# Performance work log

Measured on AMD Instinct MI355X. Metric: run time of the kernel, lower is better.

Reference implementation:

```python
import jax, jax.numpy as jnp
import numpy as np

D = 64       # d_model (channel)
NHEAD = 8    # heads in nn.MultiheadAttention
PROTO = 16   # proto_size == num_queries
EPS = 1e-5


def _haar_filters():
    L = np.array([1.0, 1.0], np.float32) / np.float32(np.sqrt(2.0))
    H = np.array([-1.0, 1.0], np.float32) / np.float32(np.sqrt(2.0))
    # WavePool: LL, LH, HL, HH Haar filters (2x2, stride 2, depthwise)
    return [jnp.asarray(np.outer(a, b)) for (a, b) in ((L, L), (L, H), (H, L), (H, H))]


def _dw(x, k2d, stride):
    # depthwise conv with the SAME 2D filter per channel; x: [B,C,H,W]
    C = x.shape[1]
    k = jnp.tile(k2d[None, None], (C, 1, 1, 1)).astype(x.dtype)
    return jax.lax.conv_general_dilated(x, k, (stride, stride), 'VALID',
        dimension_numbers=('NCHW', 'OIHW', 'NCHW'), feature_group_count=C)


def _ln(x, g, b):
    m = jnp.mean(x, -1, keepdims=True)
    v = jnp.var(x, -1, keepdims=True)
    return (x - m) * jax.lax.rsqrt(v + EPS) * g + b


def _bn(x, g, b, m, v):
    # eval-mode BatchNorm2d, x: [B,C,H,W]
    sh = (1, -1, 1, 1)
    return (x - m.reshape(sh)) * jax.lax.rsqrt(v.reshape(sh) + EPS) * g.reshape(sh) + b.reshape(sh)


def _mscw(x, lw1, lb1, lw2, lb2, gw1, gb1, gw2, gb2):
    pool = jnp.mean(x, axis=1, keepdims=True)            # [B,1,C]
    loc = jax.nn.relu(x @ lw1.T + lb1) @ lw2.T + lb2
    glo = jax.nn.relu(pool @ gw1.T + gb1) @ gw2.T + gb2
    return jax.nn.sigmoid(loc + glo)


def _mha(q, k, v, w_in, b_in, w_out, b_out):
    # standard nn.MultiheadAttention (batch_first), q:[B,Nq,D], k/v:[B,Nk,D]
    B, Nq, d = q.shape
    dk = d // NHEAD
    qp = q @ w_in[:d].T + b_in[:d]
    kp = k @ w_in[d:2 * d].T + b_in[d:2 * d]
    vp = v @ w_in[2 * d:].T + b_in[2 * d:]
    split = lambda t: t.reshape(t.shape[0], t.shape[1], NHEAD, dk).transpose(0, 2, 1, 3)
    qh, kh, vh = split(qp), split(kp), split(vp)
    scores = jnp.einsum('bhqd,bhkd->bhqk', qh, kh) * (1.0 / np.sqrt(dk))
    attn = jax.nn.softmax(scores, axis=-1)
    o = jnp.einsum('bhqk,bhkd->bhqd', attn, vh).transpose(0, 2, 1, 3).reshape(B, Nq, d)
    return o @ w_out.T + b_out


def reference(tgt, memory, pos, query_pos,
              w_in, b_in, w_out, b_out,
              ln1_g, ln1_b, ln2_g, ln2_b,
              m1_lw1, m1_lb1, m1_lw2, m1_lb2, m1_gw1, m1_gb1, m1_gw2, m1_gb2,
              m2_lw1, m2_lb1, m2_lw2, m2_lb2, m2_gw1, m2_gb1, m2_gw2, m2_gb2,
              dw_w, bn1_g, bn1_b, bn1_m, bn1_v, pw_w, bn2_g, bn2_b, bn2_m, bn2_v,
              mheads_w):
    # CrossAttentionLayer.forward_post -> custom MultiheadAttention.forward
    query = (tgt + query_pos).transpose(1, 0, 2)   # [B,Nq,C]
    key = (memory + pos).transpose(1, 0, 2)        # [B,N1,C]
    value = memory.transpose(1, 0, 2)
    B, N1, C = value.shape
    hw = int(np.sqrt(N1))
    feat = key.transpose(0, 2, 1).reshape(B, C, hw, hw)
    fLL, fLH, fHL, fHH = _haar_filters()
    LL = _dw(feat, fLL, 2)
    LH = _dw(feat, fLH, 2)
    HL = _dw(feat, fHL, 2)
    HH = _dw(feat, fHH, 2)
    high = (HL + LH + HH).reshape(B, C, -1).transpose(0, 2, 1)  # [B,N1/4,C]
    low = LL.reshape(B, C, -1).transpose(0, 2, 1)
    wei = _mscw(high + low, m1_lw1, m1_lb1, m1_lw2, m1_lb2, m1_gw1, m1_gb1, m1_gw2, m1_gb2)
    fre = wei * high + low
    x1 = _mha(query, fre, fre, w_in, b_in, w_out, b_out)
    x1 = _ln(x1 + query, ln1_g, ln1_b)
    # DSConv3x3: depthwise 3x3 + BN + ReLU, then 1x1 + BN + ReLU
    y = jax.lax.conv_general_dilated(feat, dw_w, (1, 1), ((1, 1), (1, 1)),
        dimension_numbers=('NCHW', 'OIHW', 'NCHW'), feature_group_count=C)
    y = jax.nn.relu(_bn(y, bn1_g, bn1_b, bn1_m, bn1_v))
    y = jax.lax.conv_general_dilated(y, pw_w, (1, 1), 'VALID',
        dimension_numbers=('NCHW', 'OIHW', 'NCHW'))
    y = jax.nn.relu(_bn(y, bn2_g, bn2_b, bn2_m, bn2_v))
    featf = y.reshape(B, C, -1).transpose(0, 2, 1)          # [B,N1,C]
    mw = jax.nn.softmax(featf @ mheads_w.T, axis=1)          # softmax over tokens, [B,N1,P]
    protos = jnp.einsum('bnp,bnc->bpc', mw, key)             # [B,P,C]
    attn2 = _mscw(protos + query, m2_lw1, m2_lb1, m2_lw2, m2_lb2, m2_gw1, m2_gb1, m2_gw2, m2_gb2)
    x2 = _ln(query * attn2 + query, ln2_g, ln2_b)
    return (x1 + x2).transpose(1, 0, 2)                      # [Nq,B,C]


def setup_inputs() -> dict:
    key = jax.random.key(0)
    ks = iter(jax.random.split(key, 40))
    B, HW, NQ = 8, 128, PROTO
    N1 = HW * HW
    wn = lambda *s: jax.random.normal(next(ks), s, jnp.float32) * 0.05
    inp = {
        'tgt': jax.random.normal(next(ks), (NQ, B, D), jnp.float32),
        'memory': jax.random.normal(next(ks), (N1, B, D), jnp.float32),
        'pos': jax.random.normal(next(ks), (N1, B, D), jnp.float32),
        'query_pos': jax.random.normal(next(ks), (NQ, B, D), jnp.float32),
        'w_in': wn(3 * D, D), 'b_in': jnp.zeros((3 * D,), jnp.float32),
        'w_out': wn(D, D), 'b_out': jnp.zeros((D,), jnp.float32),
        'ln1_g': jnp.ones((D,), jnp.float32), 'ln1_b': jnp.zeros((D,), jnp.float32),
        'ln2_g': jnp.ones((D,), jnp.float32), 'ln2_b': jnp.zeros((D,), jnp.float32),
        'dw_w': wn(D, 1, 3, 3),
        'bn1_g': jnp.ones((D,), jnp.float32), 'bn1_b': jnp.zeros((D,), jnp.float32),
        'bn1_m': jnp.zeros((D,), jnp.float32), 'bn1_v': jnp.ones((D,), jnp.float32),
        'pw_w': wn(D, D, 1, 1),
        'bn2_g': jnp.ones((D,), jnp.float32), 'bn2_b': jnp.zeros((D,), jnp.float32),
        'bn2_m': jnp.zeros((D,), jnp.float32), 'bn2_v': jnp.ones((D,), jnp.float32),
        'mheads_w': wn(PROTO, D),
    }
    for pfx in ('m1', 'm2'):
        for br in ('l', 'g'):
            inp[f'{pfx}_{br}w1'] = wn(D, D)
            inp[f'{pfx}_{br}b1'] = jnp.zeros((D,), jnp.float32)
            inp[f'{pfx}_{br}w2'] = wn(D, D)
            inp[f'{pfx}_{br}b2'] = jnp.zeros((D,), jnp.float32)
    return inp
```

## Files before the change

### kernel.cpp

```cpp
#include <hip/hip_runtime.h>
#include <math.h>

#define N1 16384
#define N2 4096

#define OFF_KEY   0L
#define OFF_KPH   4194304L
#define OFF_VPH   5242880L
#define OFF_WB    6291456L
#define OFF_CST   6302208L
#define OFF_POOL  6331648L
#define OFF_PROT  6332160L
#define OFF_ZZ    6340352L
#define OFF_QP    6340480L
#define OFF_QB    6348672L
#define OFF_PART  6356864L

typedef __attribute__((ext_vector_type(8))) short bf16x8;
typedef __attribute__((ext_vector_type(4))) float floatx4;

#define MFMA16(a, b, c) __builtin_amdgcn_mfma_f32_16x16x32_bf16(a, b, c, 0, 0, 0)

__device__ __forceinline__ unsigned short f2bf(float f) {
    union { float f; unsigned u; } v; v.f = f;
    unsigned r = v.u + 0x7fffu + ((v.u >> 16) & 1u);
    return (unsigned short)(r >> 16);
}
__device__ __forceinline__ float bf2f(unsigned short s) {
    union { unsigned u; float f; } v; v.u = ((unsigned)s) << 16;
    return v.f;
}
__device__ __forceinline__ float sigmoidf_(float x) { return 1.f / (1.f + __expf(-x)); }
__device__ __forceinline__ bf16x8 ldg8b(const unsigned short* p) { return *(const bf16x8*)p; }
__device__ __forceinline__ void unpack8(uint4 v, float* f) {
    f[0] = bf2f((unsigned short)(v.x & 0xffff)); f[1] = bf2f((unsigned short)(v.x >> 16));
    f[2] = bf2f((unsigned short)(v.y & 0xffff)); f[3] = bf2f((unsigned short)(v.y >> 16));
    f[4] = bf2f((unsigned short)(v.z & 0xffff)); f[5] = bf2f((unsigned short)(v.z >> 16));
    f[6] = bf2f((unsigned short)(v.w & 0xffff)); f[7] = bf2f((unsigned short)(v.w >> 16));
}

__global__ __launch_bounds__(256) void k_prep(const float* __restrict__ m1lw1,
                                              const float* __restrict__ m1lw2,
                                              const float* __restrict__ w_in,
                                              const float* __restrict__ pw,
                                              const float* __restrict__ mh,
                                              const float* __restrict__ dw_w,
                                              const float* __restrict__ bn1_g, const float* __restrict__ bn1_b,
                                              const float* __restrict__ bn1_m, const float* __restrict__ bn1_v,
                                              const float* __restrict__ bn2_g, const float* __restrict__ bn2_b,
                                              const float* __restrict__ bn2_m, const float* __restrict__ bn2_v,
                                              const float* __restrict__ m1gw1, const float* __restrict__ m1gw2,
                                              const float* __restrict__ m2gw1, const float* __restrict__ m2gw2,
                                              const float* __restrict__ m2lw1, const float* __restrict__ m2lw2,
                                              const float* __restrict__ w_out,
                                              const float* __restrict__ tgt, const float* __restrict__ qpos,
                                              const float* __restrict__ b_in,
                                              unsigned short* __restrict__ wb,
                                              float* __restrict__ cst,
                                              float* __restrict__ qp, float* __restrict__ queryb) {
    int blk = blockIdx.x, tid = threadIdx.x;
    if (blk < 84) {
        int i = blk * 256 + tid;
        float v;
        if (i < 4096) v = m1lw1[i];
        else if (i < 8192) v = m1lw2[i - 4096];
        else if (i < 16384) v = w_in[4096 + (i - 8192)];
        else if (i < 20480) v = pw[i - 16384];
        else v = mh[i - 20480];
        wb[i] = f2bf(v);
    } else if (blk < 199) {
        int j = (blk - 84) * 256 + tid;
        float v;
        if (j < 576) {
            int k = j >> 6, c = j & 63;
            float s1 = bn1_g[c] * rsqrtf(bn1_v[c] + 1e-5f);
            v = dw_w[c * 9 + k] * s1;
        } else if (j < 640) {
            int c = j - 576;
            float s1 = bn1_g[c] * rsqrtf(bn1_v[c] + 1e-5f);
            v = bn1_b[c] - bn1_m[c] * s1;
        } else if (j < 704) {
            int c = j - 640;
            v = bn2_g[c] * rsqrtf(bn2_v[c] + 1e-5f);
        } else if (j < 768) {
            int c = j - 704;
            float s2 = bn2_g[c] * rsqrtf(bn2_v[c] + 1e-5f);
            v = bn2_b[c] - bn2_m[c] * s2;
        } else {
            int jj = j - 768;
            int m = jj >> 12, idx = jj & 4095;
            int sidx = (idx & 63) * 64 + (idx >> 6);
            const float* src;
            switch (m) {
                case 0: src = m1gw1; break;
                case 1: src = m1gw2; break;
                case 2: src = m2gw1; break;
                case 3: src = m2gw2; break;
                case 4: src = m2lw1; break;
                case 5: src = m2lw2; break;
                default: src = w_out; break;
            }
            v = src[sidx];
        }
        cst[j] = v;
    } else {
        __shared__ float qv[4][64];
        int g = tid >> 6, lane = tid & 63;
        int u = (blk - 199) * 4 + g;
        int b = u >> 4, q = u & 15;
        long src = ((long)q * 8 + b) * 64 + lane;
        float v = tgt[src] + qpos[src];
        qv[g][lane] = v;
        queryb[(b * 16 + q) * 64 + lane] = v;
        __syncthreads();
        float acc = b_in[lane];
        for (int cc = 0; cc < 64; cc++) acc += qv[g][cc] * w_in[lane * 64 + cc];
        qp[(b * 16 + q) * 64 + lane] = acc;
    }
}

__global__ __launch_bounds__(256) void k_key(const float* __restrict__ mem,
                                             const float* __restrict__ pos,
                                             unsigned short* __restrict__ key,
                                             float* __restrict__ pool1raw) {
    __shared__ float sh[16][64];
    int tid = threadIdx.x;
    int b = blockIdx.x >> 9;
    int n_base = (blockIdx.x & 511) * 32;
    int c8 = tid & 7, local_n = tid >> 3;
    int n = n_base + local_n;
    long s4 = ((long)n * 8 + b) * 16 + c8 * 2;
    float4 m0 = ((const float4*)mem)[s4], m1 = ((const float4*)mem)[s4 + 1];
    float4 p0 = ((const float4*)pos)[s4], p1 = ((const float4*)pos)[s4 + 1];
    float f[8];
    f[0] = m0.x + p0.x; f[1] = m0.y + p0.y; f[2] = m0.z + p0.z; f[3] = m0.w + p0.w;
    f[4] = m1.x + p1.x; f[5] = m1.y + p1.y; f[6] = m1.z + p1.z; f[7] = m1.w + p1.w;
    uint4 o;
    o.x = (unsigned)f2bf(f[0]) | ((unsigned)f2bf(f[1]) << 16);
    o.y = (unsigned)f2bf(f[2]) | ((unsigned)f2bf(f[3]) << 16);
    o.z = (unsigned)f2bf(f[4]) | ((unsigned)f2bf(f[5]) << 16);
    o.w = (unsigned)f2bf(f[6]) | ((unsigned)f2bf(f[7]) << 16);
    ((uint4*)key)[(long)(b * 16384 + n) * 8 + c8] = o;
    int parity = (n_base >> 7) & 1;
    if (parity) {
        if (local_n & 1) {
            #pragma unroll
            for (int j = 0; j < 8; j++) sh[local_n >> 1][c8 * 8 + j] = f[j];
        }
        __syncthreads();
        if (tid < 64) {
            float s = 0.f;
            #pragma unroll
            for (int k = 0; k < 16; k++) s += sh[k][tid];
            atomicAdd(pool1raw + b * 64 + tid, s);
        }
    }
}

__global__ __launch_bounds__(256) void k_mscw1(
        const unsigned short* __restrict__ keyb, const float* __restrict__ pool1raw,
        const float* __restrict__ lb1, const float* __restrict__ lb2,
        const float* __restrict__ gb1, const float* __restrict__ gb2,
        const float* __restrict__ b_in, const unsigned short* __restrict__ wb,
        const float* __restrict__ cst,
        unsigned short* __restrict__ kph, unsigned short* __restrict__ vph) {
    __shared__ __align__(16) short stage[256 * 72];
    __shared__ __align__(16) short hbuf[64 * 72];
    __shared__ __align__(16) short wbuf[64 * 72];
    __shared__ float parr[64], gtmp[64], gbuf[64];
    int tid = threadIdx.x;
    int w = tid >> 6, l = tid & 63;
    int b = blockIdx.x >> 6, tile = blockIdx.x & 63;
    int m0 = w * 16, trow = l & 15, oct = l >> 4;
    const float* gw1T = cst + 768;
    const float* gw2T = cst + 4864;
    if (tid < 64) parr[tid] = pool1raw[b * 64 + tid] * (2.0f / 4096.0f);
    const unsigned short* src = keyb + ((long)b * 16384 + tile * 256) * 64;
    #pragma unroll
    for (int k = 0; k < 8; k++) {
        int u = k * 256 + tid;
        int p = u >> 3, o = u & 7;
        uint4 v = *(const uint4*)(src + (long)u * 8);
        *(uint4*)(stage + p * 72 + o * 8) = v;
    }
    __syncthreads();
    if (tid < 64) {
        float a = gb1[tid];
        for (int cc = 0; cc < 64; cc++) a += parr[cc] * gw1T[cc * 64 + tid];
        gtmp[tid] = fmaxf(a, 0.f);
    }
    int j = m0 + trow;
    float x[16], S[16];
    bf16x8 ax[2];
    #pragma unroll
    for (int half = 0; half < 2; half++) {
        int o = oct + half * 4;
        uint4 fa4 = *(const uint4*)(stage + (2 * j) * 72 + o * 8);
        uint4 fb4 = *(const uint4*)(stage + (2 * j + 1) * 72 + o * 8);
        uint4 fc4 = *(const uint4*)(stage + (128 + 2 * j) * 72 + o * 8);
        uint4 fd4 = *(const uint4*)(stage + (129 + 2 * j) * 72 + o * 8);
        float A[8], B[8], C[8], D[8];
        unpack8(fa4, A); unpack8(fb4, B); unpack8(fc4, C); unpack8(fd4, D);
        #pragma unroll
        for (int jj = 0; jj < 8; jj++) {
            float xd = 2.f * D[jj];
            x[half * 8 + jj] = xd;
            S[half * 8 + jj] = 0.5f * (A[jj] + B[jj] + C[jj] + D[jj]);
            ax[half][jj] = (short)f2bf(xd);
        }
    }
    const unsigned short* w1b = wb;
    const unsigned short* w2b = wb + 4096;
    const unsigned short* wkb = wb + 8192;
    const unsigned short* wvb = wb + 12288;
    #pragma unroll
    for (int t4 = 0; t4 < 4; t4++) {
        int n = t4 * 16 + trow;
        float bias = lb1[n];
        floatx4 acc = {bias, bias, bias, bias};
        acc = MFMA16(ax[0], ldg8b(w1b + n * 64 + oct * 8), acc);
        acc = MFMA16(ax[1], ldg8b(w1b + n * 64 + 32 + oct * 8), acc);
        #pragma unroll
        for (int r = 0; r < 4; r++)
            hbuf[(m0 + oct * 4 + r) * 72 + n] = (short)f2bf(fmaxf(acc[r], 0.f));
    }
    __syncthreads();
    if (tid < 64) {
        float g = gb2[tid];
        for (int hh = 0; hh < 64; hh++) g += gtmp[hh] * gw2T[hh * 64 + tid];
        gbuf[tid] = g;
    }
    __syncthreads();
    {
        bf16x8 ah0 = *(const bf16x8*)(hbuf + (m0 + trow) * 72 + oct * 8);
        bf16x8 ah1 = *(const bf16x8*)(hbuf + (m0 + trow) * 72 + 32 + oct * 8);
        #pragma unroll
        for (int t4 = 0; t4 < 4; t4++) {
            int n = t4 * 16 + trow;
            float bias = lb2[n];
            floatx4 acc = {bias, bias, bias, bias};
            acc = MFMA16(ah0, ldg8b(w2b + n * 64 + oct * 8), acc);
            acc = MFMA16(ah1, ldg8b(w2b + n * 64 + 32 + oct * 8), acc);
            float g = gbuf[n];
            #pragma unroll
            for (int r = 0; r < 4; r++)
                wbuf[(m0 + oct * 4 + r) * 72 + n] = (short)f2bf(sigmoidf_(acc[r] + g));
        }
    }
    __syncthreads();
    bf16x8 af0, af1;
    {
        bf16x8 w0 = *(const bf16x8*)(wbuf + (m0 + trow) * 72 + oct * 8);
        bf16x8 w1v = *(const bf16x8*)(wbuf + (m0 + trow) * 72 + 32 + oct * 8);
        #pragma unroll
        for (int jj = 0; jj < 8; jj++) {
            float we0 = bf2f((unsigned short)w0[jj]);
            float we1 = bf2f((unsigned short)w1v[jj]);
            af0[jj] = (short)f2bf(we0 * x[jj] + (1.f - we0) * S[jj]);
            af1[jj] = (short)f2bf(we1 * x[8 + jj] + (1.f - we1) * S[8 + jj]);
        }
    }
    __syncthreads();
    short* kbuf = hbuf; short* vbuf = wbuf;
    #pragma unroll
    for (int t4 = 0; t4 < 4; t4++) {
        int ko = t4 * 16 + trow;
        float bk = b_in[64 + ko], bv = b_in[128 + ko];
        floatx4 ak = {bk, bk, bk, bk};
        floatx4 av = {bv, bv, bv, bv};
        ak = MFMA16(af0, ldg8b(wkb + ko * 64 + oct * 8), ak);
        ak = MFMA16(af1, ldg8b(wkb + ko * 64 + 32 + oct * 8), ak);
        av = MFMA16(af0, ldg8b(wvb + ko * 64 + oct * 8), av);
        av = MFMA16(af1, ldg8b(wvb + ko * 64 + 32 + oct * 8), av);
        #pragma unroll
        for (int r = 0; r < 4; r++) {
            int row = m0 + oct * 4 + r;
            kbuf[row * 72 + ko] = (short)f2bf(ak[r]);
            vbuf[row * 72 + ko] = (short)f2bf(av[r]);
        }
    }
    __syncthreads();
    for (int u = tid; u < 512; u += 256) {
        int h = u >> 6, tok = u & 63;
        uint4 kk = *(const uint4*)(kbuf + tok * 72 + h * 8);
        uint4 vv = *(const uint4*)(vbuf + tok * 72 + h * 8);
        long du = (long)(b * 8 + h) * 4096 + tile * 64 + tok;
        ((uint4*)kph)[du] = kk;
        ((uint4*)vph)[du] = vv;
    }
}

__global__ __launch_bounds__(512) void k_dsconv(
        const unsigned short* __restrict__ keyb,
        const unsigned short* __restrict__ wb,
        const float* __restrict__ cst,
        float* __restrict__ protos, float* __restrict__ Z) {
    __shared__ __align__(16) short stage[3 * 128 * 72];
    __shared__ __align__(16) short pbuf[16 * 136];
    __shared__ float cbuf[768];
    __shared__ float zred[8][16];
    int tid = threadIdx.x;
    int w = tid >> 6, l = tid & 63;
    int b = blockIdx.x >> 7, h = blockIdx.x & 127;
    int p0 = w * 16, pr = l & 15, oct = l >> 4;
    for (int k = tid; k < 768; k += 512) cbuf[k] = cst[k];
    const unsigned short* kb = keyb + (long)b * 1048576;
    #pragma unroll
    for (int r = 0; r < 3; r++) {
        int row = h - 1 + r;
        if ((unsigned)row < 128u) {
            const unsigned short* src = kb + (long)row * 8192;
            #pragma unroll
            for (int k = 0; k < 4; k++) {
                int u = k * 512 + tid;
                int p = u >> 3, o = u & 7;
                uint4 v = *(const uint4*)(src + (long)u * 8);
                *(uint4*)(stage + (r * 128 + p) * 72 + o * 8) = v;
            }
        } else {
            uint4 zz = {0u, 0u, 0u, 0u};
            #pragma unroll
            for (int k = 0; k < 4; k++) {
                int u = k * 512 + tid;
                int p = u >> 3, o = u & 7;
                *(uint4*)(stage + (r * 128 + p) * 72 + o * 8) = zz;
            }
        }
    }
    __syncthreads();
    float accf[2][8];
    #pragma unroll
    for (int half = 0; half < 2; half++)
        #pragma unroll
        for (int jj = 0; jj < 8; jj++) accf[half][jj] = 0.f;
    #pragma unroll
    for (int r = 0; r < 3; r++) {
        #pragma unroll
        for (int kk = 0; kk < 3; kk++) {
            int col = p0 + pr - 1 + kk;
            if ((unsigned)col < 128u) {
                #pragma unroll
                for (int half = 0; half < 2; half++) {
                    int o = oct + half * 4;
                    uint4 d4 = *(const uint4*)(stage + (r * 128 + col) * 72 + o * 8);
                    float f[8]; unpack8(d4, f);
                    float4 wa = *(const float4*)(cbuf + (r * 3 + kk) * 64 + o * 8);
                    float4 wc = *(const float4*)(cbuf + (r * 3 + kk) * 64 + o * 8 + 4);
                    accf[half][0] += f[0] * wa.x; accf[half][1] += f[1] * wa.y;
                    accf[half][2] += f[2] * wa.z; accf[half][3] += f[3] * wa.w;
                    accf[half][4] += f[4] * wc.x; accf[half][5] += f[5] * wc.y;
                    accf[half][6] += f[6] * wc.z; accf[half][7] += f[7] * wc.w;
                }
            }
        }
    }
    bf16x8 af[2];
    #pragma unroll
    for (int half = 0; half < 2; half++) {
        int o = oct + half * 4;
        float4 oa = *(const float4*)(cbuf + 576 + o * 8);
        float4 ob = *(const float4*)(cbuf + 576 + o * 8 + 4);
        af[half][0] = (short)f2bf(fmaxf(accf[half][0] + oa.x, 0.f));
        af[half][1] = (short)f2bf(fmaxf(accf[half][1] + oa.y, 0.f));
        af[half][2] = (short)f2bf(fmaxf(accf[half][2] + oa.z, 0.f));
        af[half][3] = (short)f2bf(fmaxf(accf[half][3] + oa.w, 0.f));
        af[half][4] = (short)f2bf(fmaxf(accf[half][4] + ob.x, 0.f));
        af[half][5] = (short)f2bf(fmaxf(accf[half][5] + ob.y, 0.f));
        af[half][6] = (short)f2bf(fmaxf(accf[half][6] + ob.z, 0.f));
        af[half][7] = (short)f2bf(fmaxf(accf[half][7] + ob.w, 0.f));
    }
    __syncthreads();
    short* y2buf = stage;
    short* KT = stage + 18432;
    {
        const unsigned short* pwb = wb + 16384;
        #pragma unroll
        for (int t4 = 0; t4 < 4; t4++) {
            int n = t4 * 16 + pr;
            floatx4 acc = {0.f, 0.f, 0.f, 0.f};
            acc = MFMA16(af[0], ldg8b(pwb + n * 64 + oct * 8), acc);
            acc = MFMA16(af[1], ldg8b(pwb + n * 64 + 32 + oct * 8), acc);
            float s2 = cbuf[640 + n], o2 = cbuf[704 + n];
            #pragma unroll
            for (int r = 0; r < 4; r++)
                y2buf[(p0 + oct * 4 + r) * 72 + n] = (short)f2bf(fmaxf(acc[r] * s2 + o2, 0.f));
        }
        #pragma unroll
        for (int k = 0; k < 2; k++) {
            int u = k * 512 + tid;
            int n = u >> 3, o = u & 7;
            uint4 v = *(const uint4*)(stage + (128 + n) * 72 + o * 8);
            int nx = n ^ (o << 3);
            KT[(o * 8 + 0) * 136 + nx] = (short)(v.x & 0xffff);
            KT[(o * 8 + 1) * 136 + nx] = (short)(v.x >> 16);
            KT[(o * 8 + 2) * 136 + nx] = (short)(v.y & 0xffff);
            KT[(o * 8 + 3) * 136 + nx] = (short)(v.y >> 16);
            KT[(o * 8 + 4) * 136 + nx] = (short)(v.z & 0xffff);
            KT[(o * 8 + 5) * 136 + nx] = (short)(v.z >> 16);
            KT[(o * 8 + 6) * 136 + nx] = (short)(v.w & 0xffff);
            KT[(o * 8 + 7) * 136 + nx] = (short)(v.w >> 16);
        }
    }
    __syncthreads();
    {
        const unsigned short* mhb = wb + 20480;
        bf16x8 a0 = *(const bf16x8*)(y2buf + (p0 + pr) * 72 + oct * 8);
        bf16x8 a1 = *(const bf16x8*)(y2buf + (p0 + pr) * 72 + 32 + oct * 8);
        floatx4 lg = {0.f, 0.f, 0.f, 0.f};
        lg = MFMA16(a0, ldg8b(mhb + pr * 64 + oct * 8), lg);
        lg = MFMA16(a1, ldg8b(mhb + pr * 64 + 32 + oct * 8), lg);
        float zs = 0.f;
        #pragma unroll
        for (int r = 0; r < 4; r++) {
            float e = __expf(lg[r]);
            zs += e;
            pbuf[pr * 136 + p0 + oct * 4 + r] = (short)f2bf(e);
        }
        zs += __shfl_xor(zs, 16);
        zs += __shfl_xor(zs, 32);
        if (l < 16) zred[w][l] = zs;
    }
    __syncthreads();
    if (w < 4) {
        int ct = w;
        int c = ct * 16 + pr;
        int xrc = ((c >> 3) & 7) << 3;
        floatx4 acc = {0.f, 0.f, 0.f, 0.f};
        #pragma unroll
        for (int s = 0; s < 4; s++) {
            bf16x8 A = *(const bf16x8*)(pbuf + pr * 136 + s * 32 + oct * 8);
            bf16x8 B = *(const bf16x8*)(KT + c * 136 + ((s * 32 + oct * 8) ^ xrc));
            acc = MFMA16(A, B, acc);
        }
        #pragma unroll
        for (int r = 0; r < 4; r++)
            atomicAdd(protos + (b * 16 + oct * 4 + r) * 64 + c, acc[r]);
    }
    if (tid < 16) {
        float zt = 0.f;
        #pragma unroll
        for (int ww = 0; ww < 8; ww++) zt += zred[ww][tid];
        atomicAdd(Z + b * 16 + tid, zt);
    }
}

__global__ __launch_bounds__(256) void k_mha(const float* __restrict__ qp,
                                             const unsigned short* __restrict__ kph,
                                             const unsigned short* __restrict__ vph,
                                             float* __restrict__ part) {
    int bh = blockIdx.x >> 3, seg = blockIdx.x & 7;
    int b = bh >> 3, hh = bh & 7;
    int tid = threadIdx.x;
    int q = tid >> 4, sub = tid & 15;
    const float* qv = qp + (long)(b * 16 + q) * 64 + hh * 8;
    float4 q0 = ((const float4*)qv)[0];
    float4 q1 = ((const float4*)qv)[1];
    const uint4* K4 = (const uint4*)kph + (long)bh * 4096;
    const uint4* V4 = (const uint4*)vph + (long)bh * 4096;
    const float scale = 0.35355339059327373f;
    float m = -1e30f, lsum = 0.f;
    float acc[8];
    #pragma unroll
    for (int d = 0; d < 8; d++) acc[d] = 0.f;
    for (int i = 0; i < 32; i++) {
        int n = seg * 512 + i * 16 + sub;
        float k8[8]; unpack8(K4[n], k8);
        float s = q0.x * k8[0] + q0.y * k8[1] + q0.z * k8[2] + q0.w * k8[3]
                + q1.x * k8[4] + q1.y * k8[5] + q1.z * k8[6] + q1.w * k8[7];
        s *= scale;
        float nm = fmaxf(m, s);
        float corr = __expf(m - nm);
        float wgt = __expf(s - nm);
        lsum = lsum * corr + wgt;
        float v8[8]; unpack8(V4[n], v8);
        #pragma unroll
// ... 133 lines not shown
    const float* bn1_v     = (const float*)d_in[16];
    const float* pw_w      = (const float*)d_in[17];
    const float* bn2_g     = (const float*)d_in[18];
    const float* bn2_b     = (const float*)d_in[19];
    const float* bn2_m     = (const float*)d_in[20];
    const float* bn2_v     = (const float*)d_in[21];
    const float* mheads    = (const float*)d_in[22];
    const float* m1_lw1 = (const float*)d_in[23];
    const float* m1_lb1 = (const float*)d_in[24];
    const float* m1_lw2 = (const float*)d_in[25];
    const float* m1_lb2 = (const float*)d_in[26];
    const float* m1_gw1 = (const float*)d_in[27];
    const float* m1_gb1 = (const float*)d_in[28];
    const float* m1_gw2 = (const float*)d_in[29];
    const float* m1_gb2 = (const float*)d_in[30];
    const float* m2_lw1 = (const float*)d_in[31];
    const float* m2_lb1 = (const float*)d_in[32];
    const float* m2_lw2 = (const float*)d_in[33];
    const float* m2_lb2 = (const float*)d_in[34];
    const float* m2_gw1 = (const float*)d_in[35];
    const float* m2_gb1 = (const float*)d_in[36];
    const float* m2_gw2 = (const float*)d_in[37];
    const float* m2_gb2 = (const float*)d_in[38];

    float* ws = (float*)d_ws;
    float* out = (float*)d_out;
    unsigned short* keyb = (unsigned short*)(ws + OFF_KEY);
    unsigned short* kph  = (unsigned short*)(ws + OFF_KPH);
    unsigned short* vph  = (unsigned short*)(ws + OFF_VPH);
    unsigned short* wb   = (unsigned short*)(ws + OFF_WB);

    hipMemsetAsync(ws + OFF_POOL, 0, 8832 * sizeof(float), stream);

    k_prep<<<231, 256, 0, stream>>>(m1_lw1, m1_lw2, w_in, pw_w, mheads, dw_w,
                                    bn1_g, bn1_b, bn1_m, bn1_v,
                                    bn2_g, bn2_b, bn2_m, bn2_v,
                                    m1_gw1, m1_gw2, m2_gw1, m2_gw2,
                                    m2_lw1, m2_lw2, w_out,
                                    tgt, query_pos, b_in,
                                    wb, ws + OFF_CST, ws + OFF_QP, ws + OFF_QB);
    k_key<<<4096, 256, 0, stream>>>(memory, pos, keyb, ws + OFF_POOL);
    k_mscw1<<<512, 256, 0, stream>>>(keyb, ws + OFF_POOL, m1_lb1, m1_lb2,
                                     m1_gb1, m1_gb2, b_in, wb, ws + OFF_CST, kph, vph);
    k_dsconv<<<1024, 512, 0, stream>>>(keyb, wb, ws + OFF_CST,
                                       ws + OFF_PROT, ws + OFF_ZZ);
    k_mha<<<512, 256, 0, stream>>>(ws + OFF_QP, kph, vph, ws + OFF_PART);
    k_final<<<8, 1024, 0, stream>>>(ws + OFF_QB, ws + OFF_PROT, ws + OFF_ZZ, ws + OFF_PART,
                                    ws + OFF_CST, b_out,
                                    ln1_g, ln1_b, ln2_g, ln2_b,
                                    m2_lb1, m2_lb2, m2_gb1, m2_gb2,
                                    out);
}
```

Measured before the change: 247.7 us.

## Merge independent prep/key and mscw1/dsconv kernels into two horizontally fused launches

Combines k_prep and k_key into one launch, with blocks selected by block index, and combines k_mscw1 and k_dsconv into one 512-thread launch whose two roles share one shared-memory buffer. The mscw1 path is re-split so each pair of waves handles one 16-row tile across two channel halves. The goal is fewer launches and kernel boundaries, and letting the independent stages overlap on the GPU. The cost is a larger shared-memory footprint per block for the mscw1 path, which may lower occupancy. The k_stage1 key path reads pool and uses cst and wb only in later launches, so ordering across launches still holds.

```diff
diff --git a/kernel.cpp b/kernel.cpp
--- a/kernel.cpp
+++ b/kernel.cpp
@@ -39,26 +39,60 @@
     f[6] = bf2f((unsigned short)(v.w & 0xffff)); f[7] = bf2f((unsigned short)(v.w >> 16));
 }
 
-__global__ __launch_bounds__(256) void k_prep(const float* __restrict__ m1lw1,
-                                              const float* __restrict__ m1lw2,
-                                              const float* __restrict__ w_in,
-                                              const float* __restrict__ pw,
-                                              const float* __restrict__ mh,
-                                              const float* __restrict__ dw_w,
-                                              const float* __restrict__ bn1_g, const float* __restrict__ bn1_b,
-                                              const float* __restrict__ bn1_m, const float* __restrict__ bn1_v,
-                                              const float* __restrict__ bn2_g, const float* __restrict__ bn2_b,
-                                              const float* __restrict__ bn2_m, const float* __restrict__ bn2_v,
-                                              const float* __restrict__ m1gw1, const float* __restrict__ m1gw2,
-                                              const float* __restrict__ m2gw1, const float* __restrict__ m2gw2,
-                                              const float* __restrict__ m2lw1, const float* __restrict__ m2lw2,
-                                              const float* __restrict__ w_out,
-                                              const float* __restrict__ tgt, const float* __restrict__ qpos,
-                                              const float* __restrict__ b_in,
-                                              unsigned short* __restrict__ wb,
-                                              float* __restrict__ cst,
-                                              float* __restrict__ qp, float* __restrict__ queryb) {
-    int blk = blockIdx.x, tid = threadIdx.x;
+__global__ __launch_bounds__(256) void k_stage1(
+        const float* __restrict__ mem, const float* __restrict__ pos,
+        const float* __restrict__ m1lw1, const float* __restrict__ m1lw2,
+        const float* __restrict__ w_in, const float* __restrict__ pw,
+        const float* __restrict__ mh, const float* __restrict__ dw_w,
+        const float* __restrict__ bn1_g, const float* __restrict__ bn1_b,
+        const float* __restrict__ bn1_m, const float* __restrict__ bn1_v,
+        const float* __restrict__ bn2_g, const float* __restrict__ bn2_b,
+        const float* __restrict__ bn2_m, const float* __restrict__ bn2_v,
+        const float* __restrict__ m1gw1, const float* __restrict__ m1gw2,
+        const float* __restrict__ m2gw1, const float* __restrict__ m2gw2,
+        const float* __restrict__ m2lw1, const float* __restrict__ m2lw2,
+        const float* __restrict__ w_out,
+        const float* __restrict__ tgt, const float* __restrict__ qpos,
+        const float* __restrict__ b_in,
+        unsigned short* __restrict__ key, float* __restrict__ pool1raw,
+        unsigned short* __restrict__ wb, float* __restrict__ cst,
+        float* __restrict__ qp, float* __restrict__ queryb) {
+    int tid = threadIdx.x;
+    if (blockIdx.x < 4096) {
+        __shared__ float sh[16][64];
+        int b = blockIdx.x >> 9;
+        int n_base = (blockIdx.x & 511) * 32;
+        int c8 = tid & 7, local_n = tid >> 3;
+        int n = n_base + local_n;
+        long s4 = ((long)n * 8 + b) * 16 + c8 * 2;
+        float4 m0 = ((const float4*)mem)[s4], m1 = ((const float4*)mem)[s4 + 1];
+        float4 p0 = ((const float4*)pos)[s4], p1 = ((const float4*)pos)[s4 + 1];
+        float f[8];
+        f[0] = m0.x + p0.x; f[1] = m0.y + p0.y; f[2] = m0.z + p0.z; f[3] = m0.w + p0.w;
+        f[4] = m1.x + p1.x; f[5] = m1.y + p1.y; f[6] = m1.z + p1.z; f[7] = m1.w + p1.w;
+        uint4 o;
+        o.x = (unsigned)f2bf(f[0]) | ((unsigned)f2bf(f[1]) << 16);
+        o.y = (unsigned)f2bf(f[2]) | ((unsigned)f2bf(f[3]) << 16);
+        o.z = (unsigned)f2bf(f[4]) | ((unsigned)f2bf(f[5]) << 16);
+        o.w = (unsigned)f2bf(f[6]) | ((unsigned)f2bf(f[7]) << 16);
+        ((uint4*)key)[(long)(b * 16384 + n) * 8 + c8] = o;
+        int parity = (n_base >> 7) & 1;
+        if (parity) {
+            if (local_n & 1) {
+                #pragma unroll
+                for (int j = 0; j < 8; j++) sh[local_n >> 1][c8 * 8 + j] = f[j];
+            }
+            __syncthreads();
+            if (tid < 64) {
+                float s = 0.f;
+                #pragma unroll
+                for (int k = 0; k < 16; k++) s += sh[k][tid];
+                atomicAdd(pool1raw + b * 64 + tid, s);
+            }
+        }
+        return;
+    }
+    int blk = blockIdx.x - 4096;
     if (blk < 84) {
         int i = blk * 256 + tid;
         float v;
@@ -119,328 +153,293 @@
     }
 }
 
-__global__ __launch_bounds__(256) void k_key(const float* __restrict__ mem,
-                                             const float* __restrict__ pos,
-                                             unsigned short* __restrict__ key,
-                                             float* __restrict__ pool1raw) {
-    __shared__ float sh[16][64];
-    int tid = threadIdx.x;
-    int b = blockIdx.x >> 9;
-    int n_base = (blockIdx.x & 511) * 32;
-    int c8 = tid & 7, local_n = tid >> 3;
-    int n = n_base + local_n;
-    long s4 = ((long)n * 8 + b) * 16 + c8 * 2;
-    float4 m0 = ((const float4*)mem)[s4], m1 = ((const float4*)mem)[s4 + 1];
-    float4 p0 = ((const float4*)pos)[s4], p1 = ((const float4*)pos)[s4 + 1];
-    float f[8];
-    f[0] = m0.x + p0.x; f[1] = m0.y + p0.y; f[2] = m0.z + p0.z; f[3] = m0.w + p0.w;
-    f[4] = m1.x + p1.x; f[5] = m1.y + p1.y; f[6] = m1.z + p1.z; f[7] = m1.w + p1.w;
-    uint4 o;
-    o.x = (unsigned)f2bf(f[0]) | ((unsigned)f2bf(f[1]) << 16);
-    o.y = (unsigned)f2bf(f[2]) | ((unsigned)f2bf(f[3]) << 16);
-    o.z = (unsigned)f2bf(f[4]) | ((unsigned)f2bf(f[5]) << 16);
-    o.w = (unsigned)f2bf(f[6]) | ((unsigned)f2bf(f[7]) << 16);
-    ((uint4*)key)[(long)(b * 16384 + n) * 8 + c8] = o;
-    int parity = (n_base >> 7) & 1;
-    if (parity) {
-        if (local_n & 1) {
-            #pragma unroll
-            for (int j = 0; j < 8; j++) sh[local_n >> 1][c8 * 8 + j] = f[j];
-        }
-        __syncthreads();
-        if (tid < 64) {
-            float s = 0.f;
-            #pragma unroll
-            for (int k = 0; k < 16; k++) s += sh[k][tid];
-            atomicAdd(pool1raw + b * 64 + tid, s);
-        }
-    }
-}
-
-__global__ __launch_bounds__(256) void k_mscw1(
-        const unsigned short* __restrict__ keyb, const float* __restrict__ pool1raw,
+__global__ __launch_bounds__(512) void k_stage2(
+        const unsigned short* __restrict__ keyb,
+        const float* __restrict__ pool1raw,
         const float* __restrict__ lb1, const float* __restrict__ lb2,
         const float* __restrict__ gb1, const float* __restrict__ gb2,
-        const float* __restrict__ b_in, const unsigned short* __restrict__ wb,
+        const float* __restrict__ b_in,
+        const unsigned short* __restrict__ wb,
         const float* __restrict__ cst,
-        unsigned short* __restrict__ kph, unsigned short* __restrict__ vph) {
-    __shared__ __align__(16) short stage[256 * 72];
-    __shared__ __align__(16) short hbuf[64 * 72];
-    __shared__ __align__(16) short wbuf[64 * 72];
-    __shared__ float parr[64], gtmp[64], gbuf[64];
+        unsigned short* __restrict__ kph, unsigned short* __restrict__ vph,
+        float* __restrict__ protos, float* __restrict__ Z) {
+    __shared__ __align__(16) char smem[63488];
     int tid = threadIdx.x;
     int w = tid >> 6, l = tid & 63;
-    int b = blockIdx.x >> 6, tile = blockIdx.x & 63;
-    int m0 = w * 16, trow = l & 15, oct = l >> 4;
-    const float* gw1T = cst + 768;
-    const float* gw2T = cst + 4864;
-    if (tid < 64) parr[tid] = pool1raw[b * 64 + tid] * (2.0f / 4096.0f);
-    const unsigned short* src = keyb + ((long)b * 16384 + tile * 256) * 64;
-    #pragma unroll
-    for (int k = 0; k < 8; k++) {
-        int u = k * 256 + tid;
-        int p = u >> 3, o = u & 7;
-        uint4 v = *(const uint4*)(src + (long)u * 8);
-        *(uint4*)(stage + p * 72 + o * 8) = v;
-    }
-    __syncthreads();
-    if (tid < 64) {
-        float a = gb1[tid];
-        for (int cc = 0; cc < 64; cc++) a += parr[cc] * gw1T[cc * 64 + tid];
-        gtmp[tid] = fmaxf(a, 0.f);
-    }
-    int j = m0 + trow;
-    float x[16], S[16];
-    bf16x8 ax[2];
-    #pragma unroll
-    for (int half = 0; half < 2; half++) {
-        int o = oct + half * 4;
-        uint4 fa4 = *(const uint4*)(stage + (2 * j) * 72 + o * 8);
-        uint4 fb4 = *(const uint4*)(stage + (2 * j + 1) * 72 + o * 8);
-        uint4 fc4 = *(const uint4*)(stage + (128 + 2 * j) * 72 + o * 8);
-        uint4 fd4 = *(const uint4*)(stage + (129 + 2 * j) * 72 + o * 8);
-        float A[8], B[8], C[8], D[8];
-        unpack8(fa4, A); unpack8(fb4, B); unpack8(fc4, C); unpack8(fd4, D);
-        #pragma unroll
-        for (int jj = 0; jj < 8; jj++) {
-            float xd = 2.f * D[jj];
-            x[half * 8 + jj] = xd;
-            S[half * 8 + jj] = 0.5f * (A[jj] + B[jj] + C[jj] + D[jj]);
-            ax[half][jj] = (short)f2bf(xd);
-        }
-    }
-    const unsigned short* w1b = wb;
-    const unsigned short* w2b = wb + 4096;
-    const unsigned short* wkb = wb + 8192;
-    const unsigned short* wvb = wb + 12288;
-    #pragma unroll
-    for (int t4 = 0; t4 < 4; t4++) {
-        int n = t4 * 16 + trow;
-        float bias = lb1[n];
-        floatx4 acc = {bias, bias, bias, bias};
-        acc = MFMA16(ax[0], ldg8b(w1b + n * 64 + oct * 8), acc);
-        acc = MFMA16(ax[1], ldg8b(w1b + n * 64 + 32 + oct * 8), acc);
-        #pragma unroll
-        for (int r = 0; r < 4; r++)
-            hbuf[(m0 + oct * 4 + r) * 72 + n] = (short)f2bf(fmaxf(acc[r], 0.f));
-    }
-    __syncthreads();
-    if (tid < 64) {
-        float g = gb2[tid];
-        for (int hh = 0; hh < 64; hh++) g += gtmp[hh] * gw2T[hh * 64 + tid];
-        gbuf[tid] = g;
-    }
-    __syncthreads();
+    if (blockIdx.x < 512) {
+        short* stage = (short*)smem;
+        short* hbuf  = (short*)(smem + 36864);
+        short* wbuf  = (short*)(smem + 46080);
+        float* parr  = (float*)(smem + 55296);
+        float* gtmp  = parr + 64;
+        float* gbuf  = parr + 128;
+        int b = blockIdx.x >> 6, tile = blockIdx.x & 63;
+        int pairw = w >> 1, ch2 = w & 1;
+        int m0 = pairw * 16, trow = l & 15, oct = l >> 4;
+        const float* gw1T = cst + 768;
+        const float* gw2T = cst + 4864;
+        if (tid < 64) parr[tid] = pool1raw[b * 64 + tid] * (2.0f / 4096.0f);
+        const unsigned short* src = keyb + ((long)b * 16384 + tile * 256) * 64;
+        #pragma unroll
+        for (int k = 0; k < 4; k++) {
+            int u = k * 512 + tid;
+            int p = u >> 3, o = u & 7;
+            uint4 v = *(const uint4*)(src + (long)u * 8);
+            *(uint4*)(stage + p * 72 + o * 8) = v;
+        }
+        __syncthreads();
+        if (tid < 64) {
+            float a = gb1[tid];
+            for (int cc = 0; cc < 64; cc++) a += parr[cc] * gw1T[cc * 64 + tid];
+            gtmp[tid] = fmaxf(a, 0.f);
+        }
+        int j = m0 + trow;
+        float x[16], S[16];
+        bf16x8 ax[2];
+        #pragma unroll
+        for (int half = 0; half < 2; half++) {
+            int o = oct + half * 4;
+            uint4 fa4 = *(const uint4*)(stage + (2 * j) * 72 + o * 8);
+            uint4 fb4 = *(const uint4*)(stage + (2 * j + 1) * 72 + o * 8);
+            uint4 fc4 = *(const uint4*)(stage + (128 + 2 * j) * 72 + o * 8);
+            uint4 fd4 = *(const uint4*)(stage + (129 + 2 * j) * 72 + o * 8);
+            float A[8], B[8], C[8], D[8];
+            unpack8(fa4, A); unpack8(fb4, B); unpack8(fc4, C); unpack8(fd4, D);
+            #pragma unroll
+            for (int jj = 0; jj < 8; jj++) {
+                float xd = 2.f * D[jj];
+                x[half * 8 + jj] = xd;
+                S[half * 8 + jj] = 0.5f * (A[jj] + B[jj] + C[jj] + D[jj]);
+                ax[half][jj] = (short)f2bf(xd);
+            }
+        }
+        const unsigned short* w1b = wb;
+        const unsigned short* w2b = wb + 4096;
+        const unsigned short* wkb = wb + 8192;
+        const unsigned short* wvb = wb + 12288;
+        #pragma unroll
+        for (int t4i = 0; t4i < 2; t4i++) {
+            int n = (ch2 * 2 + t4i) * 16 + trow;
+            float bias = lb1[n];
+            floatx4 acc = {bias, bias, bias, bias};
+            acc = MFMA16(ax[0], ldg8b(w1b + n * 64 + oct * 8), acc);
+            acc = MFMA16(ax[1], ldg8b(w1b + n * 64 + 32 + oct * 8), acc);
+            #pragma unroll
+            for (int r = 0; r < 4; r++)
+                hbuf[(m0 + oct * 4 + r) * 72 + n] = (short)f2bf(fmaxf(acc[r], 0.f));
+        }
+        __syncthreads();
+        if (tid < 64) {
+            float g = gb2[tid];
+            for (int hh = 0; hh < 64; hh++) g += gtmp[hh] * gw2T[hh * 64 + tid];
+            gbuf[tid] = g;
+        }
+        __syncthreads();
+        {
+            bf16x8 ah0 = *(const bf16x8*)(hbuf + (m0 + trow) * 72 + oct * 8);
+            bf16x8 ah1 = *(const bf16x8*)(hbuf + (m0 + trow) * 72 + 32 + oct * 8);
+            #pragma unroll
+            for (int t4i = 0; t4i < 2; t4i++) {
+                int n = (ch2 * 2 + t4i) * 16 + trow;
+                float bias = lb2[n];
+                floatx4 acc = {bias, bias, bias, bias};
+                acc = MFMA16(ah0, ldg8b(w2b + n * 64 + oct * 8), acc);
+                acc = MFMA16(ah1, ldg8b(w2b + n * 64 + 32 + oct * 8), acc);
+                float g = gbuf[n];
+                #pragma unroll
+                for (int r = 0; r < 4; r++)
+                    wbuf[(m0 + oct * 4 + r) * 72 + n] = (short)f2bf(sigmoidf_(acc[r] + g));
+            }
+        }
+        __syncthreads();
+        bf16x8 af0, af1;
+        {
+            bf16x8 w0 = *(const bf16x8*)(wbuf + (m0 + trow) * 72 + oct * 8);
+            bf16x8 w1v = *(const bf16x8*)(wbuf + (m0 + trow) * 72 + 32 + oct * 8);
+            #pragma unroll
+            for (int jj = 0; jj < 8; jj++) {
+                float we0 = bf2f((unsigned short)w0[jj]);
+                float we1 = bf2f((unsigned short)w1v[jj]);
+                af0[jj] = (short)f2bf(we0 * x[jj] + (1.f - we0) * S[jj]);
+                af1[jj] = (short)f2bf(we1 * x[8 + jj] + (1.f - we1) * S[8 + jj]);
+            }
+        }
+        __syncthreads();
+        short* kbuf = hbuf; short* vbuf = wbuf;
+        #pragma unroll
+        for (int t4i = 0; t4i < 2; t4i++) {
+            int ko = (ch2 * 2 + t4i) * 16 + trow;
+            float bk = b_in[64 + ko], bv = b_in[128 + ko];
+            floatx4 ak = {bk, bk, bk, bk};
+            floatx4 av = {bv, bv, bv, bv};
+            ak = MFMA16(af0, ldg8b(wkb + ko * 64 + oct * 8), ak);
+            ak = MFMA16(af1, ldg8b(wkb + ko * 64 + 32 + oct * 8), ak);
+            av = MFMA16(af0, ldg8b(wvb + ko * 64 + oct * 8), av);
+            av = MFMA16(af1, ldg8b(wvb + ko * 64 + 32 + oct * 8), av);
+            #pragma unroll
+            for (int r = 0; r < 4; r++) {
+                int row = m0 + oct * 4 + r;
+                kbuf[row * 72 + ko] = (short)f2bf(ak[r]);
+                vbuf[row * 72 + ko] = (short)f2bf(av[r]);
+            }
+        }
+        __syncthreads();
+        {
+            int h = tid >> 6, tok = tid & 63;
+            uint4 kk = *(const uint4*)(kbuf + tok * 72 + h * 8);
+            uint4 vv = *(const uint4*)(vbuf + tok * 72 + h * 8);
+            long du = (long)(b * 8 + h) * 4096 + tile * 64 + tok;
+            ((uint4*)kph)[du] = kk;
+            ((uint4*)vph)[du] = vv;
+        }
+        return;
+    }
     {
-        bf16x8 ah0 = *(const bf16x8*)(hbuf + (m0 + trow) * 72 + oct * 8);
-        bf16x8 ah1 = *(const bf16x8*)(hbuf + (m0 + trow) * 72 + 32 + oct * 8);
-        #pragma unroll
-        for (int t4 = 0; t4 < 4; t4++) {
-            int n = t4 * 16 + trow;
-            float bias = lb2[n];
-            floatx4 acc = {bias, bias, bias, bias};
-            acc = MFMA16(ah0, ldg8b(w2b + n * 64 + oct * 8), acc);
-            acc = MFMA16(ah1, ldg8b(w2b + n * 64 + 32 + oct * 8), acc);
-            float g = gbuf[n];
+        short* stage = (short*)smem;
+        short* pbuf  = (short*)(smem + 55296);
+        float* cbuf  = (float*)(smem + 55296 + 4352);
+        float* zred  = (float*)(smem + 55296 + 4352 + 3072);
+        int blk = blockIdx.x - 512;
+        int b = blk >> 7, h = blk & 127;
+        int p0 = w * 16, pr = l & 15, oct = l >> 4;
+        for (int k = tid; k < 768; k += 512) cbuf[k] = cst[k];
+        const unsigned short* kb = keyb + (long)b * 1048576;
+        #pragma unroll
+        for (int r = 0; r < 3; r++) {
+            int row = h - 1 + r;
+            if ((unsigned)row < 128u) {
+                const unsigned short* src = kb + (long)row * 8192;
+                #pragma unroll
+                for (int k = 0; k < 2; k++) {
+                    int u = k * 512 + tid;
+                    int p = u >> 3, o = u & 7;
+                    uint4 v = *(const uint4*)(src + (long)u * 8);
+                    *(uint4*)(stage + (r * 128 + p) * 72 + o * 8) = v;
+                }
+            } else {
+                uint4 zz = {0u, 0u, 0u, 0u};
+                #pragma unroll
+                for (int k = 0; k < 2; k++) {
+                    int u = k * 512 + tid;
+                    int p = u >> 3, o = u & 7;
+                    *(uint4*)(stage + (r * 128 + p) * 72 + o * 8) = zz;
+                }
+            }
+        }
+        __syncthreads();
+        float accf[2][8];
+        #pragma unroll
+        for (int half = 0; half < 2; half++)
+            #pragma unroll
+            for (int jj = 0; jj < 8; jj++) accf[half][jj] = 0.f;
+        #pragma unroll
+        for (int r = 0; r < 3; r++) {
+            #pragma unroll
+            for (int kk = 0; kk < 3; kk++) {
+                int col = p0 + pr - 1 + kk;
+                if ((unsigned)col < 128u) {
+                    #pragma unroll
+                    for (int half = 0; half < 2; half++) {
+                        int o = oct + half * 4;
+                        uint4 d4 = *(const uint4*)(stage + (r * 128 + col) * 72 + o * 8);
+                        float f[8]; unpack8(d4, f);
+                        float4 wa = *(const float4*)(cbuf + (r * 3 + kk) * 64 + o * 8);
+                        float4 wc = *(const float4*)(cbuf + (r * 3 + kk) * 64 + o * 8 + 4);
+                        accf[half][0] += f[0] * wa.x; accf[half][1] += f[1] * wa.y;
+                        accf[half][2] += f[2] * wa.z; accf[half][3] += f[3] * wa.w;
+                        accf[half][4] += f[4] * wc.x; accf[half][5] += f[5] * wc.y;
+                        accf[half][6] += f[6] * wc.z; accf[half][7] += f[7] * wc.w;
+                    }
+                }
+            }
+        }
+        bf16x8 af[2];
+        #pragma unroll
+        for (int half = 0; half < 2; half++) {
+            int o = oct + half * 4;
+            float4 oa = *(const float4*)(cbuf + 576 + o * 8);
+            float4 ob = *(const float4*)(cbuf + 576 + o * 8 + 4);
+            af[half][0] = (short)f2bf(fmaxf(accf[half][0] + oa.x, 0.f));
+            af[half][1] = (short)f2bf(fmaxf(accf[half][1] + oa.y, 0.f));
+            af[half][2] = (short)f2bf(fmaxf(accf[half][2] + oa.z, 0.f));
+            af[half][3] = (short)f2bf(fmaxf(accf[half][3] + oa.w, 0.f));
+            af[half][4] = (short)f2bf(fmaxf(accf[half][4] + ob.x, 0.f));
+            af[half][5] = (short)f2bf(fmaxf(accf[half][5] + ob.y, 0.f));
+            af[half][6] = (short)f2bf(fmaxf(accf[half][6] + ob.z, 0.f));
+            af[half][7] = (short)f2bf(fmaxf(accf[half][7] + ob.w, 0.f));
+        }
+        __syncthreads();
+        short* y2buf = stage;
+        short* KT = stage + 18432;
+        {
+            const unsigned short* pwb = wb + 16384;
+            #pragma unroll
+            for (int t4 = 0; t4 < 4; t4++) {
+                int n = t4 * 16 + pr;
+                floatx4 acc = {0.f, 0.f, 0.f, 0.f};
+                acc = MFMA16(af[0], ldg8b(pwb + n * 64 + oct * 8), acc);
+                acc = MFMA16(af[1], ldg8b(pwb + n * 64 + 32 + oct * 8), acc);
+                float s2 = cbuf[640 + n], o2 = cbuf[704 + n];
+                #pragma unroll
+                for (int r = 0; r < 4; r++)
+                    y2buf[(p0 + oct * 4 + r) * 72 + n] = (short)f2bf(fmaxf(acc[r] * s2 + o2, 0.f));
+            }
+            #pragma unroll
+            for (int k = 0; k < 2; k++) {
+                int u = k * 512 + tid;
+                int n = u >> 3, o = u & 7;
+                uint4 v = *(const uint4*)(stage + (128 + n) * 72 + o * 8);
+                int nx = n ^ (o << 3);
+                KT[(o * 8 + 0) * 136 + nx] = (short)(v.x & 0xffff);
+                KT[(o * 8 + 1) * 136 + nx] = (short)(v.x >> 16);
+                KT[(o * 8 + 2) * 136 + nx] = (short)(v.y & 0xffff);
+                KT[(o * 8 + 3) * 136 + nx] = (short)(v.y >> 16);
+                KT[(o * 8 + 4) * 136 + nx] = (short)(v.z & 0xffff);
+                KT[(o * 8 + 5) * 136 + nx] = (short)(v.z >> 16);
+                KT[(o * 8 + 6) * 136 + nx] = (short)(v.w & 0xffff);
+                KT[(o * 8 + 7) * 136 + nx] = (short)(v.w >> 16);
+            }
+        }
+        __syncthreads();
+        {
+            const unsigned short* mhb = wb + 20480;
+            bf16x8 a0 = *(const bf16x8*)(y2buf + (p0 + pr) * 72 + oct * 8);
+            bf16x8 a1 = *(const bf16x8*)(y2buf + (p0 + pr) * 72 + 32 + oct * 8);
+            floatx4 lg = {0.f, 0.f, 0.f, 0.f};
+            lg = MFMA16(a0, ldg8b(mhb + pr * 64 + oct * 8), lg);
+            lg = MFMA16(a1, ldg8b(mhb + pr * 64 + 32 + oct * 8), lg);
+            float zs = 0.f;
+            #pragma unroll
+            for (int r = 0; r < 4; r++) {
+                float e = __expf(lg[r]);
+                zs += e;
+                pbuf[pr * 136 + p0 + oct * 4 + r] = (short)f2bf(e);
+            }
+            zs += __shfl_xor(zs, 16);
+            zs += __shfl_xor(zs, 32);
+            if (l < 16) zred[w * 16 + l] = zs;
+        }
+        __syncthreads();
+        if (w < 4) {
+            int c = w * 16 + pr;
+            int xrc = ((c >> 3) & 7) << 3;
+            floatx4 acc = {0.f, 0.f, 0.f, 0.f};
+            #pragma unroll
+            for (int s = 0; s < 4; s++) {
+                bf16x8 A = *(const bf16x8*)(pbuf + pr * 136 + s * 32 + oct * 8);
+                bf16x8 B = *(const bf16x8*)(KT + c * 136 + ((s * 32 + oct * 8) ^ xrc));
+                acc = MFMA16(A, B, acc);
+            }
             #pragma unroll
             for (int r = 0; r < 4; r++)
-                wbuf[(m0 + oct * 4 + r) * 72 + n] = (short)f2bf(sigmoidf_(acc[r] + g));
-        }
-    }
-    __syncthreads();
-    bf16x8 af0, af1;
-    {
-        bf16x8 w0 = *(const bf16x8*)(wbuf + (m0 + trow) * 72 + oct * 8);
-        bf16x8 w1v = *(const bf16x8*)(wbuf + (m0 + trow) * 72 + 32 + oct * 8);
-        #pragma unroll
-        for (int jj = 0; jj < 8; jj++) {
-            float we0 = bf2f((unsigned short)w0[jj]);
-            float we1 = bf2f((unsigned short)w1v[jj]);
-            af0[jj] = (short)f2bf(we0 * x[jj] + (1.f - we0) * S[jj]);
-            af1[jj] = (short)f2bf(we1 * x[8 + jj] + (1.f - we1) * S[8 + jj]);
-        }
-    }
-    __syncthreads();
-    short* kbuf = hbuf; short* vbuf = wbuf;
-    #pragma unroll
-    for (int t4 = 0; t4 < 4; t4++) {
-        int ko = t4 * 16 + trow;
-        float bk = b_in[64 + ko], bv = b_in[128 + ko];
-        floatx4 ak = {bk, bk, bk, bk};
-        floatx4 av = {bv, bv, bv, bv};
-        ak = MFMA16(af0, ldg8b(wkb + ko * 64 + oct * 8), ak);
-        ak = MFMA16(af1, ldg8b(wkb + ko * 64 + 32 + oct * 8), ak);
-        av = MFMA16(af0, ldg8b(wvb + ko * 64 + oct * 8), av);
-        av = MFMA16(af1, ldg8b(wvb + ko * 64 + 32 + oct * 8), av);
-        #pragma unroll
-        for (int r = 0; r < 4; r++) {
-            int row = m0 + oct * 4 + r;
-            kbuf[row * 72 + ko] = (short)f2bf(ak[r]);
-            vbuf[row * 72 + ko] = (short)f2bf(av[r]);
-        }
-    }
-    __syncthreads();
-    for (int u = tid; u < 512; u += 256) {
-        int h = u >> 6, tok = u & 63;
-        uint4 kk = *(const uint4*)(kbuf + tok * 72 + h * 8);
-        uint4 vv = *(const uint4*)(vbuf + tok * 72 + h * 8);
-        long du = (long)(b * 8 + h) * 4096 + tile * 64 + tok;
-        ((uint4*)kph)[du] = kk;
-        ((uint4*)vph)[du] = vv;
-    }
-}
-
-__global__ __launch_bounds__(512) void k_dsconv(
-        const unsigned short* __restrict__ keyb,
-        const unsigned short* __restrict__ wb,
-        const float* __restrict__ cst,
-        float* __restrict__ protos, float* __restrict__ Z) {
-    __shared__ __align__(16) short stage[3 * 128 * 72];
-    __shared__ __align__(16) short pbuf[16 * 136];
-    __shared__ float cbuf[768];
-    __shared__ float zred[8][16];
-    int tid = threadIdx.x;
-    int w = tid >> 6, l = tid & 63;
-    int b = blockIdx.x >> 7, h = blockIdx.x & 127;
-    int p0 = w * 16, pr = l & 15, oct = l >> 4;
-    for (int k = tid; k < 768; k += 512) cbuf[k] = cst[k];
-    const unsigned short* kb = keyb + (long)b * 1048576;
-    #pragma unroll
-    for (int r = 0; r < 3; r++) {
-        int row = h - 1 + r;
-        if ((unsigned)row < 128u) {
-            const unsigned short* src = kb + (long)row * 8192;
-            #pragma unroll
-            for (int k = 0; k < 4; k++) {
-                int u = k * 512 + tid;
-                int p = u >> 3, o = u & 7;
-                uint4 v = *(const uint4*)(src + (long)u * 8);
-                *(uint4*)(stage + (r * 128 + p) * 72 + o * 8) = v;
-            }
-        } else {
-            uint4 zz = {0u, 0u, 0u, 0u};
-            #pragma unroll
-            for (int k = 0; k < 4; k++) {
-                int u = k * 512 + tid;
-                int p = u >> 3, o = u & 7;
-                *(uint4*)(stage + (r * 128 + p) * 72 + o * 8) = zz;
-            }
-        }
-    }
-    __syncthreads();
-    float accf[2][8];
-    #pragma unroll
-    for (int half = 0; half < 2; half++)
-        #pragma unroll
-        for (int jj = 0; jj < 8; jj++) accf[half][jj] = 0.f;
-    #pragma unroll
-    for (int r = 0; r < 3; r++) {
-        #pragma unroll
-        for (int kk = 0; kk < 3; kk++) {
-            int col = p0 + pr - 1 + kk;
-            if ((unsigned)col < 128u) {
-                #pragma unroll
-                for (int half = 0; half < 2; half++) {
-                    int o = oct + half * 4;
-                    uint4 d4 = *(const uint4*)(stage + (r * 128 + col) * 72 + o * 8);
-                    float f[8]; unpack8(d4, f);
-                    float4 wa = *(const float4*)(cbuf + (r * 3 + kk) * 64 + o * 8);
-                    float4 wc = *(const float4*)(cbuf + (r * 3 + kk) * 64 + o * 8 + 4);
-                    accf[half][0] += f[0] * wa.x; accf[half][1] += f[1] * wa.y;
-                    accf[half][2] += f[2] * wa.z; accf[half][3] += f[3] * wa.w;
-                    accf[half][4] += f[4] * wc.x; accf[half][5] += f[5] * wc.y;
-                    accf[half][6] += f[6] * wc.z; accf[half][7] += f[7] * wc.w;
-                }
-            }
-        }
-    }
-    bf16x8 af[2];
-    #pragma unroll
-    for (int half = 0; half < 2; half++) {
-        int o = oct + half * 4;
-        float4 oa = *(const float4*)(cbuf + 576 + o * 8);
-        float4 ob = *(const float4*)(cbuf + 576 + o * 8 + 4);
-        af[half][0] = (short)f2bf(fmaxf(accf[half][0] + oa.x, 0.f));
-        af[half][1] = (short)f2bf(fmaxf(accf[half][1] + oa.y, 0.f));
-        af[half][2] = (short)f2bf(fmaxf(accf[half][2] + oa.z, 0.f));
-        af[half][3] = (short)f2bf(fmaxf(accf[half][3] + oa.w, 0.f));
-        af[half][4] = (short)f2bf(fmaxf(accf[half][4] + ob.x, 0.f));
-        af[half][5] = (short)f2bf(fmaxf(accf[half][5] + ob.y, 0.f));
-        af[half][6] = (short)f2bf(fmaxf(accf[half][6] + ob.z, 0.f));
-        af[half][7] = (short)f2bf(fmaxf(accf[half][7] + ob.w, 0.f));
-    }
-    __syncthreads();
-    short* y2buf = stage;
-    short* KT = stage + 18432;
-    {
-        const unsigned short* pwb = wb + 16384;
-        #pragma unroll
-        for (int t4 = 0; t4 < 4; t4++) {
-            int n = t4 * 16 + pr;
-            floatx4 acc = {0.f, 0.f, 0.f, 0.f};
-            acc = MFMA16(af[0], ldg8b(pwb + n * 64 + oct * 8), acc);
-            acc = MFMA16(af[1], ldg8b(pwb + n * 64 + 32 + oct * 8), acc);
-            float s2 = cbuf[640 + n], o2 = cbuf[704 + n];
-            #pragma unroll
-            for (int r = 0; r < 4; r++)
-                y2buf[(p0 + oct * 4 + r) * 72 + n] = (short)f2bf(fmaxf(acc[r] * s2 + o2, 0.f));
-        }
-        #pragma unroll
-        for (int k = 0; k < 2; k++) {
-            int u = k * 512 + tid;
-            int n = u >> 3, o = u & 7;
-            uint4 v = *(const uint4*)(stage + (128 + n) * 72 + o * 8);
-            int nx = n ^ (o << 3);
-            KT[(o * 8 + 0) * 136 + nx] = (short)(v.x & 0xffff);
-            KT[(o * 8 + 1) * 136 + nx] = (short)(v.x >> 16);
-            KT[(o * 8 + 2) * 136 + nx] = (short)(v.y & 0xffff);
-            KT[(o * 8 + 3) * 136 + nx] = (short)(v.y >> 16);
-            KT[(o * 8 + 4) * 136 + nx] = (short)(v.z & 0xffff);
-            KT[(o * 8 + 5) * 136 + nx] = (short)(v.z >> 16);
-            KT[(o * 8 + 6) * 136 + nx] = (short)(v.w & 0xffff);
-            KT[(o * 8 + 7) * 136 + nx] = (short)(v.w >> 16);
-        }
-    }
-    __syncthreads();
-    {
-        const unsigned short* mhb = wb + 20480;
-        bf16x8 a0 = *(const bf16x8*)(y2buf + (p0 + pr) * 72 + oct * 8);
-        bf16x8 a1 = *(const bf16x8*)(y2buf + (p0 + pr) * 72 + 32 + oct * 8);
-        floatx4 lg = {0.f, 0.f, 0.f, 0.f};
-        lg = MFMA16(a0, ldg8b(mhb + pr * 64 + oct * 8), lg);
-        lg = MFMA16(a1, ldg8b(mhb + pr * 64 + 32 + oct * 8), lg);
-        float zs = 0.f;
-        #pragma unroll
-        for (int r = 0; r < 4; r++) {
-            float e = __expf(lg[r]);
-            zs += e;
-            pbuf[pr * 136 + p0 + oct * 4 + r] = (short)f2bf(e);
-        }
-        zs += __shfl_xor(zs, 16);
-        zs += __shfl_xor(zs, 32);
-        if (l < 16) zred[w][l] = zs;
-    }
-    __syncthreads();
-    if (w < 4) {
-        int ct = w;
-        int c = ct * 16 + pr;
-        int xrc = ((c >> 3) & 7) << 3;
-        floatx4 acc = {0.f, 0.f, 0.f, 0.f};
-        #pragma unroll
-        for (int s = 0; s < 4; s++) {
-            bf16x8 A = *(const bf16x8*)(pbuf + pr * 136 + s * 32 + oct * 8);
-            bf16x8 B = *(const bf16x8*)(KT + c * 136 + ((s * 32 + oct * 8) ^ xrc));
-            acc = MFMA16(A, B, acc);
-        }
-        #pragma unroll
-        for (int r = 0; r < 4; r++)
-            atomicAdd(protos + (b * 16 + oct * 4 + r) * 64 + c, acc[r]);
-    }
-    if (tid < 16) {
-        float zt = 0.f;
-        #pragma unroll
-        for (int ww = 0; ww < 8; ww++) zt += zred[ww][tid];
-        atomicAdd(Z + b * 16 + tid, zt);
+                atomicAdd(protos + (b * 16 + oct * 4 + r) * 64 + c, acc[r]);
+        }
+        if (tid < 16) {
+            float zt = 0.f;
+            #pragma unroll
+            for (int ww = 0; ww < 8; ww++) zt += zred[ww * 16 + tid];
+            atomicAdd(Z + b * 16 + tid, zt);
+        }
     }
 }
 
@@ -640,18 +639,19 @@
 
     hipMemsetAsync(ws + OFF_POOL, 0, 8832 * sizeof(float), stream);
 
-    k_prep<<<231, 256, 0, stream>>>(m1_lw1, m1_lw2, w_in, pw_w, mheads, dw_w,
-                                    bn1_g, bn1_b, bn1_m, bn1_v,
-                                    bn2_g, bn2_b, bn2_m, bn2_v,
-                                    m1_gw1, m1_gw2, m2_gw1, m2_gw2,
-                                    m2_lw1, m2_lw2, w_out,
-                                    tgt, query_pos, b_in,
-                                    wb, ws + OFF_CST, ws + OFF_QP, ws + OFF_QB);
-    k_key<<<4096, 256, 0, stream>>>(memory, pos, keyb, ws + OFF_POOL);
-    k_mscw1<<<512, 256, 0, stream>>>(keyb, ws + OFF_POOL, m1_lb1, m1_lb2,
-                                     m1_gb1, m1_gb2, b_in, wb, ws + OFF_CST, kph, vph);
-    k_dsconv<<<1024, 512, 0, stream>>>(keyb, wb, ws + OFF_CST,
-                                       ws + OFF_PROT, ws + OFF_ZZ);
+    k_stage1<<<4327, 256, 0, stream>>>(memory, pos,
+                                       m1_lw1, m1_lw2, w_in, pw_w, mheads, dw_w,
+                                       bn1_g, bn1_b, bn1_m, bn1_v,
+                                       bn2_g, bn2_b, bn2_m, bn2_v,
+                                       m1_gw1, m1_gw2, m2_gw1, m2_gw2,
+                                       m2_lw1, m2_lw2, w_out,
+                                       tgt, query_pos, b_in,
+                                       keyb, ws + OFF_POOL, wb, ws + OFF_CST,
+                                       ws + OFF_QP, ws + OFF_QB);
+    k_stage2<<<1536, 512, 0, stream>>>(keyb, ws + OFF_POOL,
+                                       m1_lb1, m1_lb2, m1_gb1, m1_gb2, b_in,
+                                       wb, ws + OFF_CST,
+                                       kph, vph, ws + OFF_PROT, ws + OFF_ZZ);
     k_mha<<<512, 256, 0, stream>>>(ws + OFF_QP, kph, vph, ws + OFF_PART);
     k_final<<<8, 1024, 0, stream>>>(ws + OFF_QB, ws + OFF_PROT, ws + OFF_ZZ, ws + OFF_PART,
                                     ws + OFF_CST, b_out,
```

Measured after the change: 243.4 us. About the same (-1.8%).
